# Performance work log

Measured on AMD Instinct MI355X. Metric: run time of the kernel, lower is better.

## Reference

```python
import jax, jax.numpy as jnp
import numpy as np

C, G, NH, NE = 640, 32, 8, 512
B, H, W, P = 8, 32, 32, 77
HD = C // NH
EPS = 1e-5


def _groupnorm(x, g, b):
    # x: (B, C, H, W); normalize over (C//G, H, W) within each of G groups
    bb, cc, hh, ww = x.shape
    xg = x.reshape(bb, G, cc // G, hh, ww)
    mu = xg.mean(axis=(2, 3, 4), keepdims=True)
    var = xg.var(axis=(2, 3, 4), keepdims=True)
    xg = (xg - mu) * jax.lax.rsqrt(var + EPS)
    return xg.reshape(bb, cc, hh, ww) * g[None, :, None, None] + b[None, :, None, None]


def _layernorm(x, g, b):
    mu = x.mean(axis=-1, keepdims=True)
    var = x.var(axis=-1, keepdims=True)
    return (x - mu) * jax.lax.rsqrt(var + EPS) * g + b


def _split_heads(t):
    # (B, S, C) -> (B, NH, S, HD)
    bb, ss, _ = t.shape
    return t.reshape(bb, ss, NH, HD).transpose(0, 2, 1, 3)


def _attn(q, k, v):
    # q,k,v: (B, NH, S, HD) — manual softmax(q k^T / sqrt(d)) v, as in the source
    scores = jnp.einsum('bhqd,bhkd->bhqk', q, k) / (HD ** 0.5)
    probs = jax.nn.softmax(scores, axis=-1)
    out = jnp.einsum('bhqk,bhkd->bhqd', probs, v)
    bb = q.shape[0]
    return out.transpose(0, 2, 1, 3).reshape(bb, q.shape[2], C)


def unet_attention_fwd(x, p, gn_g, gn_b, ci_w, ci_b, ln1_g, ln1_b,
                       qkv_w, qkv_b, saw_w, saw_b, ln2_g, ln2_b,
                       caq_w, caq_b, cak_w, cak_b, cav_w, cav_b, caw_w, caw_b,
                       ln3_g, ln3_b, g1_w, g1_b, g2_w, g2_b, co_w, co_b):
    residue_long = x
    h = _groupnorm(x, gn_g, gn_b)
    # conv_input: 1x1 conv == per-pixel linear; ci_w: (C_in, C_out)
    h = jnp.einsum('bihw,io->bohw', h, ci_w) + ci_b[None, :, None, None]
    bb, cc, hh, ww = h.shape
    h = h.reshape(bb, cc, hh * ww).transpose(0, 2, 1)  # (B, HW, C)

    # self attention
    res = h
    t = _layernorm(h, ln1_g, ln1_b)
    qkv = t @ qkv_w + qkv_b
    q, k, v = jnp.split(qkv, 3, axis=-1)
    t = _attn(_split_heads(q), _split_heads(k), _split_heads(v))
    h = res + (t @ saw_w + saw_b)

    # cross attention (prompt p: (B, 77, NE))
    res = h
    t = _layernorm(h, ln2_g, ln2_b)
    q = t @ caq_w + caq_b
    k = p @ cak_w + cak_b
    v = p @ cav_w + cav_b
    t = _attn(_split_heads(q), _split_heads(k), _split_heads(v))
    h = res + (t @ caw_w + caw_b)

    # GEGLU MLP (exact GELU, matching torch F.gelu default)
    res = h
    t = _layernorm(h, ln3_g, ln3_b)
    proj = t @ g1_w + g1_b  # (B, HW, 8C)
    a, gate = jnp.split(proj, 2, axis=-1)
    t = a * jax.nn.gelu(gate, approximate=False)
    h = res + (t @ g2_w + g2_b)

    h = h.transpose(0, 2, 1).reshape(bb, cc, hh, ww)
    out = jnp.einsum('bihw,io->bohw', h, co_w) + co_b[None, :, None, None]
    return out + residue_long


def setup_inputs() -> dict:
    keys = jax.random.split(jax.random.key(0), 20)
    ki = iter(keys)
    s = 0.02

    def w(shape):
        return jax.random.normal(next(ki), shape, jnp.float32) * s

    return {
        'x': jax.random.normal(next(ki), (B, C, H, W), jnp.float32),
        'p': jax.random.normal(next(ki), (B, P, NE), jnp.float32),
        'gn_g': jnp.ones((C,), jnp.float32), 'gn_b': jnp.zeros((C,), jnp.float32),
        'ci_w': w((C, C)), 'ci_b': jnp.zeros((C,), jnp.float32),
        'ln1_g': jnp.ones((C,), jnp.float32), 'ln1_b': jnp.zeros((C,), jnp.float32),
        'qkv_w': w((C, 3 * C)), 'qkv_b': jnp.zeros((3 * C,), jnp.float32),
        'saw_w': w((C, C)), 'saw_b': jnp.zeros((C,), jnp.float32),
        'ln2_g': jnp.ones((C,), jnp.float32), 'ln2_b': jnp.zeros((C,), jnp.float32),
        'caq_w': w((C, C)), 'caq_b': jnp.zeros((C,), jnp.float32),
        'cak_w': w((NE, C)), 'cak_b': jnp.zeros((C,), jnp.float32),
        'cav_w': w((NE, C)), 'cav_b': jnp.zeros((C,), jnp.float32),
        'caw_w': w((C, C)), 'caw_b': jnp.zeros((C,), jnp.float32),
        'ln3_g': jnp.ones((C,), jnp.float32), 'ln3_b': jnp.zeros((C,), jnp.float32),
        'g1_w': w((C, 8 * C)), 'g1_b': jnp.zeros((8 * C,), jnp.float32),
        'g2_w': w((4 * C, C)), 'g2_b': jnp.zeros((C,), jnp.float32),
        'co_w': w((C, C)), 'co_b': jnp.zeros((C,), jnp.float32),
    }


def reference(x, p, gn_g, gn_b, ci_w, ci_b, ln1_g, ln1_b,
              qkv_w, qkv_b, saw_w, saw_b, ln2_g, ln2_b,
              caq_w, caq_b, cak_w, cak_b, cav_w, cav_b, caw_w, caw_b,
              ln3_g, ln3_b, g1_w, g1_b, g2_w, g2_b, co_w, co_b):
    return unet_attention_fwd(x, p, gn_g, gn_b, ci_w, ci_b, ln1_g, ln1_b,
                              qkv_w, qkv_b, saw_w, saw_b, ln2_g, ln2_b,
                              caq_w, caq_b, cak_w, cak_b, cav_w, cav_b, caw_w, caw_b,
                              ln3_g, ln3_b, g1_w, g1_b, g2_w, g2_b, co_w, co_b)
```

## Files before the change

### kernel.cpp

```cpp
#include <hip/hip_runtime.h>
#include <math.h>

typedef unsigned short u16;
typedef __attribute__((ext_vector_type(8))) short short8;
typedef __attribute__((ext_vector_type(4))) float f32x4;

#define DI static __device__ __forceinline__

DI float bf2f(u16 u) { union { unsigned u; float f; } c; c.u = (unsigned)u << 16; return c.f; }
DI u16 f2bf(float f) {
  union { float f; unsigned u; } c; c.f = f;
  unsigned r = c.u + 0x7fffu + ((c.u >> 16) & 1u);
  return (u16)(r >> 16);
}

DI void gload16(const u16* g, u16* l) {
  __builtin_amdgcn_global_load_lds(
      (const __attribute__((address_space(1))) unsigned int*)g,
      (__attribute__((address_space(3))) unsigned int*)l, 16, 0, 0);
}

DI void xcd_swz(int& bx, int& by, int gx, int gy) {
  int id = by * gx + bx;
  int n = gx * gy;
  int q = n >> 3, r = n & 7;
  int xcd = id & 7, k = id >> 3;
  int s = (xcd < r) ? (xcd * (q + 1) + k) : (r * (q + 1) + (xcd - r) * q + k);
  bx = s % gx;
  by = s / gx;
}

DI void xcd_swz_rect(int& bx, int& by, int gx, int gy) {
  if ((gx & 7) == 0) {
    int RC = gx >> 3;
    if (RC <= 8 && (8 % RC) == 0) {
      int RR = 8 / RC;
      if ((gy % RR) == 0) {
        int id = by * gx + bx;
        int xcd = id & 7, k = id >> 3;
        int rc = xcd % RC, rr = xcd / RC;
        int RH = gy / RR;
        bx = rc * 8 + (k & 7);
        by = rr * RH + (k >> 3);
        return;
      }
    }
  }
  xcd_swz(bx, by, gx, gy);
}

DI const short8* fragp(const u16* unit, int row, int g4) {
  int off = row * 64 + g4 * 16;
  off ^= ((off >> 7) & 3) << 4;
  return (const short8*)((const char*)unit + off);
}

struct PrepDesc { const float* src; u16* dst; int K, N, nbx, boff, perm; };
struct PrepArgs { PrepDesc d[10]; };

__global__ __launch_bounds__(256) void prep_all(PrepArgs a) {
  int bid = blockIdx.x;
  int i = 0;
  while (i < 9 && bid >= a.d[i + 1].boff) i++;
  const PrepDesc D = a.d[i];
  int rel = bid - D.boff;
  int bx = rel % D.nbx, by = rel / D.nbx;
  int K = D.K, N = D.N;
  __shared__ float tile[32][33];
  int k0 = by * 32, n0 = bx * 32;
  int tid = threadIdx.x;
  int ni = tid & 31, ki8 = tid >> 5;
  for (int q = 0; q < 4; q++) {
    int k = ki8 + q * 8;
    tile[k][ni] = D.src[(size_t)(k0 + k) * N + n0 + ni];
  }
  __syncthreads();
  int kj = tid & 31, nj8 = tid >> 5;
  for (int q = 0; q < 4; q++) {
    int n = nj8 + q * 8;
    int nold = n0 + n;
    int rowp = nold;
    if (D.perm) {
      rowp = (nold < 2560) ? ((nold >> 5) * 64 + (nold & 31))
                           : (((nold - 2560) >> 5) * 64 + 32 + (nold & 31));
    }
    D.dst[(size_t)rowp * K + k0 + kj] = f2bf(tile[kj][n]);
  }
}

__global__ __launch_bounds__(256) void conv_bf16(const float* __restrict__ in,
                                                 u16* __restrict__ out, long n) {
  long i = (long)blockIdx.x * 256 + threadIdx.x;
  if (i < n) out[i] = f2bf(in[i]);
}

__global__ __launch_bounds__(256) void concat2(const float* __restrict__ a,
                                               const float* __restrict__ b,
                                               float* __restrict__ o, int n) {
  int i = blockIdx.x * 256 + threadIdx.x;
  if (i < n) o[i] = a[i];
  else if (i < 2 * n) o[i] = b[i - n];
}

__global__ __launch_bounds__(256) void gn_stats(const float* __restrict__ x,
                                                float* __restrict__ mean_o,
                                                float* __restrict__ rstd_o) {
  int bg = blockIdx.x;
  const float4* p = (const float4*)(x + (size_t)bg * 20480);
  float s = 0.f, sq = 0.f;
  for (int i = threadIdx.x; i < 5120; i += 256) {
    float4 v = p[i];
    s += v.x + v.y + v.z + v.w;
    sq += v.x * v.x + v.y * v.y + v.z * v.z + v.w * v.w;
  }
  for (int off = 1; off < 64; off <<= 1) { s += __shfl_xor(s, off); sq += __shfl_xor(sq, off); }
  __shared__ float ps[4], pq[4];
  int w = threadIdx.x >> 6;
  if ((threadIdx.x & 63) == 0) { ps[w] = s; pq[w] = sq; }
  __syncthreads();
  if (threadIdx.x == 0) {
    float S = ps[0] + ps[1] + ps[2] + ps[3];
    float Q = pq[0] + pq[1] + pq[2] + pq[3];
    float mu = S / 20480.f;
    float var = Q / 20480.f - mu * mu;
    mean_o[bg] = mu;
    rstd_o[bg] = rsqrtf(var + 1e-5f);
  }
}

__global__ __launch_bounds__(256) void gn_apply(const float* __restrict__ x,
                                                const float* __restrict__ mean_,
                                                const float* __restrict__ rstd_,
                                                const float* __restrict__ g,
                                                const float* __restrict__ bb,
                                                u16* __restrict__ out) {
  __shared__ float tile[32][33];
  int b = blockIdx.z, c0 = blockIdx.y * 32, s0 = blockIdx.x * 32;
  int tid = threadIdx.x;
  int si = tid & 31, ci8 = tid >> 5;
  for (int i = 0; i < 4; i++) {
    int c = c0 + ci8 + i * 8;
    int gg = c / 20;
    float mu = mean_[b * 32 + gg], rs = rstd_[b * 32 + gg];
    float v = x[((size_t)b * 640 + c) * 1024 + s0 + si];
    tile[ci8 + i * 8][si] = (v - mu) * rs * g[c] + bb[c];
  }
  __syncthreads();
  int cj = tid & 31, sj8 = tid >> 5;
  for (int i = 0; i < 4; i++) {
    int sj = sj8 + i * 8;
    out[((size_t)b * 1024 + s0 + sj) * 640 + c0 + cj] = f2bf(tile[cj][sj]);
  }
}

__global__ __launch_bounds__(256) void ln_kernel(const float* __restrict__ in,
                                                 const float* __restrict__ g,
                                                 const float* __restrict__ bb,
                                                 u16* __restrict__ out) {
  int t = blockIdx.x * 4 + (threadIdx.x >> 6);
  int lane = threadIdx.x & 63;
  const float* row = in + (size_t)t * 640;
  float xv[10], s = 0.f, sq = 0.f;
  for (int j = 0; j < 10; j++) {
    xv[j] = row[lane + j * 64];
    s += xv[j];
    sq += xv[j] * xv[j];
  }
  for (int off = 1; off < 64; off <<= 1) { s += __shfl_xor(s, off); sq += __shfl_xor(sq, off); }
  float mu = s * (1.f / 640.f);
  float var = sq * (1.f / 640.f) - mu * mu;
  float rstd = rsqrtf(var + 1e-5f);
  for (int j = 0; j < 10; j++) {
    int c = lane + j * 64;
    out[(size_t)t * 640 + c] = f2bf((xv[j] - mu) * rstd * g[c] + bb[c]);
  }
}

template <int MODE>
DI void store_elem(void* outp, const float* res, size_t o, float val) {
  if (MODE == 0)
    ((float*)outp)[o] = val;
  else if (MODE == 1)
    ((u16*)outp)[o] = f2bf(val);
  else if (MODE == 2)
    ((float*)outp)[o] = val + res[o];
  else
    ((u16*)outp)[o] = f2bf(val + res[o]);
}

template <int MODE>
__global__ __launch_bounds__(512, 1) void gemm256(const u16* __restrict__ A,
                                                  const u16* __restrict__ Bt,
                                                  const float* __restrict__ bias,
                                                  void* outp, const float* res,
                                                  int M, int N, int K) {
  __shared__ __align__(16) u16 As[4][8192];
  __shared__ __align__(16) u16 Bs[4][8192];
  const int tid = threadIdx.x;
  const int lane = tid & 63, wid = tid >> 6;
  const int wm = wid >> 2, wn = wid & 3;
  const int rq = lane & 15, g4 = lane >> 4;
  int bx = blockIdx.x, by = blockIdx.y;
  xcd_swz_rect(bx, by, gridDim.x, gridDim.y);
  const int m0 = bx * 256, n0 = by * 256;

  int D0 = tid * 16;
  int so = D0 ^ (((D0 >> 7) & 3) << 4);
  const int srow = so >> 6;
  const int sk16 = (so & 63) >> 1;

  f32x4 acc[8][4] = {};
  const int nt = K >> 5;

#define STG_A(kt)                                                              \
  {                                                                            \
    gload16(A + (size_t)(m0 + srow) * K + (kt)*32 + sk16,                      \
            &As[(kt) & 3][0] + tid * 8);                                       \
    gload16(A + (size_t)(m0 + 128 + srow) * K + (kt)*32 + sk16,                \
            &As[(kt) & 3][4096] + tid * 8);                                    \
  }
#define STG_B(kt)                                                              \
  {                                                                            \
    gload16(Bt + (size_t)(n0 + srow) * K + (kt)*32 + sk16,                     \
            &Bs[(kt) & 3][0] + tid * 8);                                       \
    gload16(Bt + (size_t)(n0 + 128 + srow) * K + (kt)*32 + sk16,               \
            &Bs[(kt) & 3][4096] + tid * 8);                                    \
  }
#define BAR asm volatile("s_barrier" ::: "memory")

#define PH1(T)                                                                 \
  {                                                                            \
    const u16* Au = &As[(T) & 3][0];                                           \
    const u16* Bu = &Bs[(T) & 3][0];                                           \
    _Pragma("unroll") for (int i = 0; i < 4; i++)                              \
        af[i] = *fragp(Au, wm * 128 + i * 16 + rq, g4);                        \
    _Pragma("unroll") for (int j = 0; j < 4; j++)                              \
        bf[j] = *fragp(Bu, wn * 64 + j * 16 + rq, g4);                         \
    BAR;                                                                       \
    asm volatile("s_waitcnt lgkmcnt(0)" ::: "memory");                         \
    __builtin_amdgcn_sched_barrier(0);                                         \
    __builtin_amdgcn_s_setprio(1);                                             \
    _Pragma("unroll") for (int i = 0; i < 4; i++)                              \
        _Pragma("unroll") for (int j = 0; j < 4; j++)                          \
            acc[i][j] =                                                        \
        __builtin_amdgcn_mfma_f32_16x16x32_bf16(af[i], bf[j], acc[i][j], 0, 0, 0); \
    __builtin_amdgcn_s_setprio(0);                                             \
  }

#define PH2(T, DO_STG, WSTR)                                                   \
  {                                                                            \
    const u16* Au = &As[(T) & 3][0];                                           \
    _Pragma("unroll") for (int i = 0; i < 4; i++)                              \
        af[i] = *fragp(Au, wm * 128 + 64 + i * 16 + rq, g4);                   \
    if (DO_STG) { STG_A((T) + 3); STG_B((T) + 3); }                            \
    asm volatile(WSTR ::: "memory");                                           \
    BAR;                                                                       \
    asm volatile("s_waitcnt lgkmcnt(0)" ::: "memory");                         \
    __builtin_amdgcn_sched_barrier(0);                                         \
    __builtin_amdgcn_s_setprio(1);                                             \
    _Pragma("unroll") for (int i = 0; i < 4; i++)                              \
        _Pragma("unroll") for (int j = 0; j < 4; j++)                          \
            acc[4 + i][j] =                                                    \
        __builtin_amdgcn_mfma_f32_16x16x32_bf16(af[i], bf[j], acc[4 + i][j], 0, 0, 0); \
    __builtin_amdgcn_s_setprio(0);                                             \
  }

  STG_A(0); STG_B(0); STG_A(1); STG_B(1); STG_A(2); STG_B(2);
  asm volatile("s_waitcnt vmcnt(8)" ::: "memory");
  BAR;

  short8 af[4], bf[4];
  int t = 0;
  for (; t < nt - 3; t++) {
    PH1(t);
    PH2(t, true, "s_waitcnt vmcnt(8)");
  }
  PH1(t); PH2(t, false, "s_waitcnt vmcnt(4)"); t++;
  PH1(t); PH2(t, false, "s_waitcnt vmcnt(0)"); t++;
  PH1(t); PH2(t, false, "s_nop 0");

  if (MODE == 5) {
#pragma unroll
    for (int mf = 0; mf < 8; mf++) {
      int mb = m0 + wm * 128 + mf * 16 + g4 * 4;
#pragma unroll
      for (int j = 0; j < 2; j++) {
        int n = n0 + wn * 64 + j * 16 + rq;
        int c = (n >> 6) * 32 + (n & 31);
        float ba = bias[c];
        float bg = bias[2560 + c];
#pragma unroll
        for (int r = 0; r < 4; r++) {
          float a = acc[mf][j][r] + ba;
          float gt = acc[mf][j + 2][r] + bg;
          float gl = 0.5f * gt * (1.f + erff(gt * 0.70710678f));
          ((u16*)outp)[(size_t)(mb + r) * 2560 + c] = f2bf(a * gl);
        }
      }
    }
  } else {
#pragma unroll
    for (int mf = 0; mf < 8; mf++) {
#pragma unroll
      for (int j = 0; j < 4; j++) {
        int n = n0 + wn * 64 + j * 16 + rq;
        if (n >= N) continue;
        float bv = bias[n];
        int mb = m0 + wm * 128 + mf * 16 + g4 * 4;
        f32x4 v = acc[mf][j];
#pragma unroll
        for (int r = 0; r < 4; r++) {
          size_t o = (size_t)(mb + r) * N + n;
          ((u16*)outp)[o] = f2bf(v[r] + bv);
        }
      }
    }
  }
  (void)res;
#undef STG_A
#undef STG_B
#undef PH1
#undef PH2
#undef BAR
}

template <int MODE>
__global__ __launch_bounds__(256) void gemm_bt64(const u16* __restrict__ A,
                                                 const u16* __restrict__ Bt,
                                                 const float* __restrict__ bias,
                                                 void* outp, const float* res,
                                                 int M, int N, int K) {
  __shared__ __align__(16) u16 As[4][2048];
  __shared__ __align__(16) u16 Bs[4][4096];
  const int tid = threadIdx.x;
  const int lane = tid & 63, wid = tid >> 6;
  const int wm = wid >> 1, wn = wid & 1;
  int bx = blockIdx.x, by = blockIdx.y;
  xcd_swz(bx, by, gridDim.x, gridDim.y);
  const int m0 = bx * 64, n0 = by * 128;
  const int rq = lane & 15, g4 = lane >> 4;

  int D0 = tid * 16;
  int so = D0 ^ (((D0 >> 7) & 3) << 4);
  const int srowS = so >> 6;
  const int sk16 = (so & 63) >> 1;
  int gmA = m0 + srowS;  if (gmA >= M) gmA = M - 1;
  const u16* gA = A + (size_t)gmA * K + sk16;
  const u16* gB0 = Bt + (size_t)(n0 + srowS) * K + sk16;
  const u16* gB1 = Bt + (size_t)(n0 + 64 + srowS) * K + sk16;

  f32x4 acc[2][4] = {};

  auto STAGE = [&](int buf, int k0) {
    gload16(gA + k0, &As[buf][tid * 8]);
    gload16(gB0 + k0, &Bs[buf][tid * 8]);
    gload16(gB1 + k0, &Bs[buf][2048 + tid * 8]);
  };
  auto COMPUTE = [&](int buf) {
    short8 af[2], bfr[4];
    for (int i = 0; i < 2; i++)
      af[i] = *fragp(&As[buf][0], wm * 32 + i * 16 + rq, g4);
    for (int j = 0; j < 4; j++)
      bfr[j] = *fragp(&Bs[buf][0], wn * 64 + j * 16 + rq, g4);
    __builtin_amdgcn_s_setprio(1);
    for (int i = 0; i < 2; i++)
      for (int j = 0; j < 4; j++)
        acc[i][j] = __builtin_amdgcn_mfma_f32_16x16x32_bf16(af[i], bfr[j], acc[i][j], 0, 0, 0);
    __builtin_amdgcn_s_setprio(0);
  };

  const int nk = K >> 5;
  STAGE(0, 0);
  STAGE(1, 32);
  int t = 0;
  for (; t < nk - 2; t++) {
    STAGE((t + 2) & 3, (t + 2) << 5);
    asm volatile("s_waitcnt vmcnt(6)" ::: "memory");
    __builtin_amdgcn_s_barrier();
    COMPUTE(t & 3);
  }
  asm volatile("s_waitcnt vmcnt(3)" ::: "memory");
  __builtin_amdgcn_s_barrier();
  COMPUTE(t & 3);
  t++;
  asm volatile("s_waitcnt vmcnt(0)" ::: "memory");
  __builtin_amdgcn_s_barrier();
  COMPUTE(t & 3);

  for (int j = 0; j < 4; j++) {
    int n = n0 + wn * 64 + j * 16 + rq;
    float bv = bias[n];
    for (int i = 0; i < 2; i++) {
      int mb = m0 + wm * 32 + i * 16 + g4 * 4;
      f32x4 v = acc[i][j];
      if (MODE == 3) {
        int b = mb >> 10, sp = mb & 1023;
        size_t o = ((size_t)b * 640 + n) * 1024 + sp;
        f32x4 xv = *(const f32x4*)(res + o);
        f32x4 ov;
        for (int r = 0; r < 4; r++) ov[r] = v[r] + bv + xv[r];
        *(f32x4*)((float*)outp + o) = ov;
      } else {
        for (int r = 0; r < 4; r++) {
          int m = mb + r;
          if (m >= M) break;
          store_elem<MODE>(outp, res, (size_t)m * N + n, v[r] + bv);
        }
      }
    }
  }
}

__global__ __launch_bounds__(256) void attn_kernel(const u16* __restrict__ Qb, int ldq, long qbs,
                                                   const u16* __restrict__ Kb, int ldk, long kbs,
                                                   const u16* __restrict__ Vb,
                                                   u16* __restrict__ Ob, int ldo, long obs,
                                                   int Sk, float scale) {
  __shared__ __align__(16) u16 Ks[64 * 96];
  __shared__ __align__(16) u16 Vt[80 * 64];
  __shared__ __align__(16) u16 Ps[4][16 * 72];
  const short8 zero = {0, 0, 0, 0, 0, 0, 0, 0};
  const int tid = threadIdx.x;
  const int lane = tid & 63, w = tid >> 6;
  const int rq = lane & 15, g4 = lane >> 4;
  const int b = blockIdx.z, h = blockIdx.y;
  const u16* Q = Qb + (size_t)b * qbs + h * 80;
  const u16* Kp = Kb + (size_t)b * kbs + h * 80;
  const u16* Vp = Vb + (size_t)b * kbs + h * 80;
  u16* Op = Ob + (size_t)b * obs + h * 80;
  const int q0 = blockIdx.x * 64 + w * 16;
  const float Af = scale * 1.44269504f;

  short8 qa[3];
#pragma unroll
  for (int kk = 0; kk < 3; kk++) {
    int d = kk * 32 + g4 * 8;
    qa[kk] = (d < 80) ? *(const short8*)(Q + (size_t)(q0 + rq) * ldq + d) : zero;
  }
  f32x4 oacc[5] = {};
  float m_run = -1e30f, l_run = 0.f;

  const int nkt = (Sk + 63) >> 6;
  for (int kt = 0; kt < nkt; kt++) {
    const int kbase = kt * 64;
    for (int s = tid; s < 768; s += 256) {
      int row = s / 12, c = s % 12;
      int kidx = kbase + row;
      short8 v = zero;
      if (c < 10 && kidx < Sk) v = *(const short8*)(Kp + (size_t)kidx * ldk + c * 8);
      int byte = row * 192 + c * 16;
      byte ^= (row & 7) << 4;
      *(short8*)((char*)Ks + byte) = v;
    }
    for (int s = tid; s < 320; s += 256) {
      int k2 = (s & 31) * 2, c = s >> 5;
      int k0i = kbase + k2;
      short8 v0 = zero, v1 = zero;
      if (k0i < Sk) v0 = *(const short8*)(Vp + (size_t)k0i * ldk + c * 8);
      if (k0i + 1 < Sk) v1 = *(const short8*)(Vp + (size_t)(k0i + 1) * ldk + c * 8);
#pragma unroll
      for (int jj = 0; jj < 8; jj++) {
        int d = c * 8 + jj;
        unsigned cm = (unsigned)(u16)v0[jj] | ((unsigned)(u16)v1[jj] << 16);
        int byte = d * 128 + k2 * 2;
        byte ^= (d & 7) << 4;
        *(unsigned*)((char*)Vt + byte) = cm;
      }
    }
    __syncthreads();

    f32x4 sc[4] = {};
#pragma unroll
    for (int n = 0; n < 4; n++)
#pragma unroll
      for (int kk = 0; kk < 3; kk++) {
        int row = n * 16 + rq;
        int byte = row * 192 + (kk * 32 + g4 * 8) * 2;
        byte ^= (rq & 7) << 4;
        short8 kb = *(const short8*)((const char*)Ks + byte);
        sc[n] = __builtin_amdgcn_mfma_f32_16x16x32_bf16(kb, qa[kk], sc[n], 0, 0, 0);
      }
    const bool full = (kbase + 64 <= Sk);
    if (!full) {
#pragma unroll
      for (int n = 0; n < 4; n++)
#pragma unroll
        for (int r = 0; r < 4; r++)
          if (kbase + n * 16 + g4 * 4 + r >= Sk) sc[n][r] = -1e30f;
    }
    float t0 = fmaxf(fmaxf(sc[0][0], sc[0][1]), fmaxf(sc[0][2], sc[0][3]));
    float t1 = fmaxf(fmaxf(sc[1][0], sc[1][1]), fmaxf(sc[1][2], sc[1][3]));
    float t2 = fmaxf(fmaxf(sc[2][0], sc[2][1]), fmaxf(sc[2][2], sc[2][3]));
    float t3 = fmaxf(fmaxf(sc[3][0], sc[3][1]), fmaxf(sc[3][2], sc[3][3]));
    float tm = fmaxf(fmaxf(t0, t1), fmaxf(t2, t3));
    tm = fmaxf(tm, __shfl_xor(tm, 16));
    tm = fmaxf(tm, __shfl_xor(tm, 32));
    if (!__all(tm <= m_run + 48.0f)) {
      float mn = fmaxf(m_run, tm);
      float sf = exp2f(Af * (m_run - mn));
      m_run = mn;
      l_run *= sf;
      float sfo[4];
#pragma unroll
      for (int r = 0; r < 4; r++) sfo[r] = __shfl(sf, g4 * 4 + r);
#pragma unroll
      for (int nn = 0; nn < 5; nn++)
#pragma unroll
        for (int r = 0; r < 4; r++) oacc[nn][r] *= sfo[r];
    }
    const float Am = Af * m_run;
    float rs0 = 0.f, rs1 = 0.f;
#pragma unroll
    for (int n = 0; n < 4; n++) {
      float p0 = exp2f(fmaf(Af, sc[n][0], -Am));
      float p1 = exp2f(fmaf(Af, sc[n][1], -Am));
      float p2 = exp2f(fmaf(Af, sc[n][2], -Am));
      float p3 = exp2f(fmaf(Af, sc[n][3], -Am));
      sc[n][0] = p0; sc[n][1] = p1; sc[n][2] = p2; sc[n][3] = p3;
      rs0 += p0 + p1;
      rs1 += p2 + p3;
    }
    float rsum = rs0 + rs1;
    rsum += __shfl_xor(rsum, 16);
    rsum += __shfl_xor(rsum, 32);
    l_run += rsum;
#pragma unroll
    for (int n = 0; n < 4; n++) {
      unsigned pk0, pk1;
      asm("v_cvt_pk_bf16_f32 %0, %1, %2" : "=v"(pk0) : "v"(sc[n][0]), "v"(sc[n][1]));
      asm("v_cvt_pk_bf16_f32 %0, %1, %2" : "=v"(pk1) : "v"(sc[n][2]), "v"(sc[n][3]));
      int base = rq * 72 + n * 16 + g4 * 4;
      *(unsigned*)&Ps[w][base] = pk0;
      *(unsigned*)&Ps[w][base + 2] = pk1;
    }
    __builtin_amdgcn_s_setprio(1);
#pragma unroll
    for (int s = 0; s < 2; s++) {
      short8 pa = *(const short8*)&Ps[w][rq * 72 + s * 32 + g4 * 8];
#pragma unroll
      for (int nn = 0; nn < 5; nn++) {
        int row = nn * 16 + rq;
        int byte = row * 128 + (s * 32 + g4 * 8) * 2;
        byte ^= (rq & 7) << 4;
        short8 vb = *(const short8*)((const char*)Vt + byte);
        oacc[nn] = __builtin_amdgcn_mfma_f32_16x16x32_bf16(pa, vb, oacc[nn], 0, 0, 0);
      }
    }
    __builtin_amdgcn_s_setprio(0);
    __syncthreads();
  }
  float lo[4];
#pragma unroll
  for (int r = 0; r < 4; r++) lo[r] = 1.0f / __shfl(l_run, g4 * 4 + r);
#pragma unroll
  for (int nn = 0; nn < 5; nn++)
#pragma unroll
    for (int r = 0; r < 4; r++)
      Op[(size_t)(q0 + g4 * 4 + r) * ldo + nn * 16 + rq] = f2bf(oacc[nn][r] * lo[r]);
}

extern "C" void kernel_launch(void* const* d_in, const int* in_sizes, int n_in,
                              void* d_out, int out_size, void* d_ws, size_t ws_size,
                              hipStream_t stream) {
  (void)in_sizes; (void)n_in; (void)out_size; (void)ws_size;
  const float* x = (const float*)d_in[0];
  const float* p = (const float*)d_in[1];
  const float* gn_g = (const float*)d_in[2];
  const float* gn_b = (const float*)d_in[3];
  const float* ci_w = (const float*)d_in[4];
  const float* ci_b = (const float*)d_in[5];
  const float* ln1_g = (const float*)d_in[6];
  const float* ln1_b = (const float*)d_in[7];
  const float* qkv_w = (const float*)d_in[8];
  const float* qkv_b = (const float*)d_in[9];
  const float* saw_w = (const float*)d_in[10];
  const float* saw_b = (const float*)d_in[11];
  const float* ln2_g = (const float*)d_in[12];
  const float* ln2_b = (const float*)d_in[13];
  const float* caq_w = (const float*)d_in[14];
  const float* caq_b = (const float*)d_in[15];
  const float* cak_w = (const float*)d_in[16];
  const float* cak_b = (const float*)d_in[17];
  const float* cav_w = (const float*)d_in[18];
  const float* cav_b = (const float*)d_in[19];
  const float* caw_w = (const float*)d_in[20];
  const float* caw_b = (const float*)d_in[21];
  const float* ln3_g = (const float*)d_in[22];
  const float* ln3_b = (const float*)d_in[23];
  const float* g1_w = (const float*)d_in[24];
  const float* g1_b = (const float*)d_in[25];
  const float* g2_w = (const float*)d_in[26];
  const float* g2_b = (const float*)d_in[27];
  const float* co_w = (const float*)d_in[28];
  const float* co_b = (const float*)d_in[29];
  float* out = (float*)d_out;

  char* ws = (char*)d_ws;
  size_t off = 0;
  auto alloc = [&](size_t bytes) {
    size_t o = off;
    off += (bytes + 255) & ~(size_t)255;
    return o;
  };
  u16* WCI = (u16*)(ws + alloc((size_t)768 * 640 * 2));
  u16* WQKV = (u16*)(ws + alloc((size_t)2048 * 640 * 2));
  u16* WSAW = (u16*)(ws + alloc((size_t)768 * 640 * 2));
  u16* WCAQ = (u16*)(ws + alloc((size_t)768 * 640 * 2));
  u16* WCAKV = (u16*)(ws + alloc((size_t)1280 * 512 * 2));
  u16* WCAW = (u16*)(ws + alloc((size_t)768 * 640 * 2));
  u16* WG1 = (u16*)(ws + alloc((size_t)5120 * 640 * 2));
  u16* WG2 = (u16*)(ws + alloc((size_t)768 * 2560 * 2));
  u16* WCO = (u16*)(ws + alloc((size_t)768 * 640 * 2));
  u16* X = (u16*)(ws + alloc((size_t)8192 * 640 * 2));
  u16* Y = (u16*)(ws + alloc((size_t)8192 * 640 * 2));
  float* F1 = (float*)(ws + alloc((size_t)8192 * 640 * 4));
  u16* QKV = (u16*)(ws + alloc((size_t)8192 * 1920 * 2));
  u16* PBF = (u16*)(ws + alloc((size_t)616 * 512 * 2));
  u16* KVC = (u16*)(ws + alloc((size_t)616 * 1280 * 2));
  u16* TG = (u16*)(ws + alloc((size_t)8192 * 2560 * 2));
  float* GNM = (float*)(ws + alloc(256 * 4));
  float* GNR = (float*)(ws + alloc(256 * 4));
  float* CBIAS = (float*)(ws + alloc(1280 * 4));

  PrepArgs pa;
  int boff = 0;
  auto addw = [&](int idx, const float* src, u16* dst, int K, int N, int perm) {
    pa.d[idx].src = src; pa.d[idx].dst = dst;
    pa.d[idx].K = K; pa.d[idx].N = N;
    pa.d[idx].nbx = N / 32; pa.d[idx].boff = boff; pa.d[idx].perm = perm;
    boff += (N / 32) * (K / 32);
  };
  addw(0, ci_w, WCI, 640, 640, 0);
  addw(1, qkv_w, WQKV, 640, 1920, 0);
  addw(2, saw_w, WSAW, 640, 640, 0);
  addw(3, caq_w, WCAQ, 640, 640, 0);
  addw(4, cak_w, WCAKV, 512, 640, 0);
  addw(5, cav_w, WCAKV + (size_t)640 * 512, 512, 640, 0);
  addw(6, caw_w, WCAW, 640, 640, 0);
  addw(7, g1_w, WG1, 640, 5120, 1);
  addw(8, g2_w, WG2, 2560, 640, 0);
  addw(9, co_w, WCO, 640, 640, 0);
  prep_all<<<boff, 256, 0, stream>>>(pa);
  conv_bf16<<<1232, 256, 0, stream>>>(p, PBF, (long)616 * 512);
  concat2<<<5, 256, 0, stream>>>(cak_b, cav_b, CBIAS, 640);

  gn_stats<<<256, 256, 0, stream>>>(x, GNM, GNR);
  gn_apply<<<dim3(32, 20, 8), 256, 0, stream>>>(x, GNM, GNR, gn_g, gn_b, X);

  const float scale = 0.11180339887498949f;

  gemm_bt64<0><<<dim3(128, 5), 256, 0, stream>>>(X, WCI, ci_b, F1, nullptr, 8192, 640, 640);
  ln_kernel<<<2048, 256, 0, stream>>>(F1, ln1_g, ln1_b, Y);
  gemm256<1><<<dim3(32, 8), 512, 0, stream>>>(Y, WQKV, qkv_b, QKV, nullptr, 8192, 1920, 640);
  attn_kernel<<<dim3(16, 8, 8), 256, 0, stream>>>(QKV, 1920, (long)1024 * 1920,
                                                  QKV + 640, 1920, (long)1024 * 1920,
                                                  QKV + 1280, X, 640, (long)1024 * 640,
                                                  1024, scale);
  gemm_bt64<2><<<dim3(128, 5), 256, 0, stream>>>(X, WSAW, saw_b, F1, F1, 8192, 640, 640);
  ln_kernel<<<2048, 256, 0, stream>>>(F1, ln2_g, ln2_b, Y);
  gemm_bt64<1><<<dim3(128, 5), 256, 0, stream>>>(Y, WCAQ, caq_b, X, nullptr, 8192, 640, 640);
  gemm_bt64<1><<<dim3(10, 10), 256, 0, stream>>>(PBF, WCAKV, CBIAS, KVC, nullptr, 616, 1280, 512);
  attn_kernel<<<dim3(16, 8, 8), 256, 0, stream>>>(X, 640, (long)1024 * 640,
                                                  KVC, 1280, (long)77 * 1280,
                                                  KVC + 640, Y, 640, (long)1024 * 640,
                                                  77, scale);
  gemm_bt64<2><<<dim3(128, 5), 256, 0, stream>>>(Y, WCAW, caw_b, F1, F1, 8192, 640, 640);
  ln_kernel<<<2048, 256, 0, stream>>>(F1, ln3_g, ln3_b, X);
  gemm256<5><<<dim3(32, 20), 512, 0, stream>>>(X, WG1, g1_b, TG, nullptr, 8192, 5120, 640);
  gemm_bt64<4><<<dim3(128, 5), 256, 0, stream>>>(TG, WG2, g2_b, X, F1, 8192, 640, 2560);
  gemm_bt64<3><<<dim3(128, 5), 256, 0, stream>>>(X, WCO, co_b, out, x, 8192, 640, 640);
}
```

Measured before the change: 445.2 us.

## Run GEGLU GEMM on new 128x128 tile kernel with supertile block swizzle

Adds a gemm_bt kernel that uses 128x128 tiles, 256 threads, a 4-buffer LDS ring and a fused GEGLU epilogue. It replaces the 256-tile, 512-thread gemm256 for the large G1 projection. Blocks are remapped into 8x8 supertiles to improve L2 reuse of A and B. The GEGLU epilogue is removed from gemm256, trading larger-tile reuse for more blocks and a simpler pipeline.

```diff
diff --git a/kernel.cpp b/kernel.cpp
--- a/kernel.cpp
+++ b/kernel.cpp
@@ -45,6 +45,19 @@
         return;
       }
     }
+  }
+  xcd_swz(bx, by, gx, gy);
+}
+
+DI void supertile_swz(int& bx, int& by, int gx, int gy) {
+  if ((gx & 7) == 0 && (gy & 7) == 0) {
+    int id = by * gx + bx;
+    int s = id >> 6, w = id & 63;
+    int syn = gy >> 3;
+    int sy = s % syn, sx = s / syn;
+    bx = sx * 8 + (w & 7);
+    by = sy * 8 + (w >> 3);
+    return;
   }
   xcd_swz(bx, by, gx, gy);
 }
@@ -279,40 +292,19 @@
   PH1(t); PH2(t, false, "s_waitcnt vmcnt(0)"); t++;
   PH1(t); PH2(t, false, "s_nop 0");
 
-  if (MODE == 5) {
-#pragma unroll
-    for (int mf = 0; mf < 8; mf++) {
+#pragma unroll
+  for (int mf = 0; mf < 8; mf++) {
+#pragma unroll
+    for (int j = 0; j < 4; j++) {
+      int n = n0 + wn * 64 + j * 16 + rq;
+      if (n >= N) continue;
+      float bv = bias[n];
       int mb = m0 + wm * 128 + mf * 16 + g4 * 4;
-#pragma unroll
-      for (int j = 0; j < 2; j++) {
-        int n = n0 + wn * 64 + j * 16 + rq;
-        int c = (n >> 6) * 32 + (n & 31);
-        float ba = bias[c];
-        float bg = bias[2560 + c];
-#pragma unroll
-        for (int r = 0; r < 4; r++) {
-          float a = acc[mf][j][r] + ba;
-          float gt = acc[mf][j + 2][r] + bg;
-          float gl = 0.5f * gt * (1.f + erff(gt * 0.70710678f));
-          ((u16*)outp)[(size_t)(mb + r) * 2560 + c] = f2bf(a * gl);
-        }
-      }
-    }
-  } else {
-#pragma unroll
-    for (int mf = 0; mf < 8; mf++) {
-#pragma unroll
-      for (int j = 0; j < 4; j++) {
-        int n = n0 + wn * 64 + j * 16 + rq;
-        if (n >= N) continue;
-        float bv = bias[n];
-        int mb = m0 + wm * 128 + mf * 16 + g4 * 4;
-        f32x4 v = acc[mf][j];
-#pragma unroll
-        for (int r = 0; r < 4; r++) {
-          size_t o = (size_t)(mb + r) * N + n;
-          ((u16*)outp)[o] = f2bf(v[r] + bv);
-        }
+      f32x4 v = acc[mf][j];
+#pragma unroll
+      for (int r = 0; r < 4; r++) {
+        size_t o = (size_t)(mb + r) * N + n;
+        ((u16*)outp)[o] = f2bf(v[r] + bv);
       }
     }
   }
@@ -322,6 +314,117 @@
 #undef PH1
 #undef PH2
 #undef BAR
+}
+
+template <int MODE>
+__global__ __launch_bounds__(256) void gemm_bt(const u16* __restrict__ A,
+                                               const u16* __restrict__ Bt,
+                                               const float* __restrict__ bias,
+                                               void* outp, const float* res,
+                                               int M, int N, int K) {
+  __shared__ __align__(16) u16 As[4][4096];
+  __shared__ __align__(16) u16 Bs[4][4096];
+  const int tid = threadIdx.x;
+  const int lane = tid & 63, wid = tid >> 6;
+  const int wm = wid >> 1, wn = wid & 1;
+  int bx = blockIdx.x, by = blockIdx.y;
+  supertile_swz(bx, by, gridDim.x, gridDim.y);
+  const int m0 = bx * 128, n0 = by * 128;
+  const int rq = lane & 15, g4 = lane >> 4;
+
+  int D0 = tid * 16;
+  int so = D0 ^ (((D0 >> 7) & 3) << 4);
+  const int srowS = so >> 6;
+  const int sk16 = (so & 63) >> 1;
+  int gmA0 = m0 + srowS;       if (gmA0 >= M) gmA0 = M - 1;
+  int gmA1 = m0 + 64 + srowS;  if (gmA1 >= M) gmA1 = M - 1;
+  const u16* gA0 = A + (size_t)gmA0 * K + sk16;
+  const u16* gA1 = A + (size_t)gmA1 * K + sk16;
+  const u16* gB0 = Bt + (size_t)(n0 + srowS) * K + sk16;
+  const u16* gB1 = Bt + (size_t)(n0 + 64 + srowS) * K + sk16;
+
+  f32x4 acc[4][4] = {};
+
+  auto STAGE = [&](int buf, int k0) {
+    gload16(gA0 + k0, &As[buf][tid * 8]);
+    gload16(gA1 + k0, &As[buf][2048 + tid * 8]);
+    gload16(gB0 + k0, &Bs[buf][tid * 8]);
+    gload16(gB1 + k0, &Bs[buf][2048 + tid * 8]);
+  };
+  auto COMPUTE = [&](int buf) {
+    short8 af[4], bfr[4];
+    for (int i = 0; i < 4; i++)
+      af[i] = *fragp(&As[buf][0], wm * 64 + i * 16 + rq, g4);
+    for (int j = 0; j < 4; j++)
+      bfr[j] = *fragp(&Bs[buf][0], wn * 64 + j * 16 + rq, g4);
+    __builtin_amdgcn_s_setprio(1);
+    for (int i = 0; i < 4; i++)
+      for (int j = 0; j < 4; j++)
+        acc[i][j] = __builtin_amdgcn_mfma_f32_16x16x32_bf16(af[i], bfr[j], acc[i][j], 0, 0, 0);
+    __builtin_amdgcn_s_setprio(0);
+  };
+
+  const int nk = K >> 5;
+  STAGE(0, 0);
+  STAGE(1, 32);
+  int t = 0;
+  for (; t < nk - 2; t++) {
+    STAGE((t + 2) & 3, (t + 2) << 5);
+    asm volatile("s_waitcnt vmcnt(8)" ::: "memory");
+    __builtin_amdgcn_s_barrier();
+    COMPUTE(t & 3);
+  }
+  asm volatile("s_waitcnt vmcnt(4)" ::: "memory");
+  __builtin_amdgcn_s_barrier();
+  COMPUTE(t & 3);
+  t++;
+  asm volatile("s_waitcnt vmcnt(0)" ::: "memory");
+  __builtin_amdgcn_s_barrier();
+  COMPUTE(t & 3);
+
+  if (MODE == 5) {
+#pragma unroll
+    for (int i = 0; i < 4; i++) {
+      int mb = m0 + wm * 64 + i * 16 + g4 * 4;
+#pragma unroll
+      for (int j = 0; j < 2; j++) {
+        int n = n0 + wn * 64 + j * 16 + rq;
+        int c = (n >> 6) * 32 + (n & 31);
+        float ba = bias[c];
+        float bg = bias[2560 + c];
+#pragma unroll
+        for (int r = 0; r < 4; r++) {
+          float a = acc[i][j][r] + ba;
+          float gt = acc[i][j + 2][r] + bg;
+          float gl = 0.5f * gt * (1.f + erff(gt * 0.70710678f));
+          ((u16*)outp)[(size_t)(mb + r) * 2560 + c] = f2bf(a * gl);
+        }
+      }
+    }
+    return;
+  }
+  for (int j = 0; j < 4; j++) {
+    int n = n0 + wn * 64 + j * 16 + rq;
+    float bv = bias[n];
+    for (int i = 0; i < 4; i++) {
+      int mb = m0 + wm * 64 + i * 16 + g4 * 4;
+      f32x4 v = acc[i][j];
+      if (MODE == 3) {
+        int b = mb >> 10, sp = mb & 1023;
+        size_t o = ((size_t)b * 640 + n) * 1024 + sp;
+        f32x4 xv = *(const f32x4*)(res + o);
+        f32x4 ov;
+        for (int r = 0; r < 4; r++) ov[r] = v[r] + bv + xv[r];
+        *(f32x4*)((float*)outp + o) = ov;
+      } else {
+        for (int r = 0; r < 4; r++) {
+          int m = mb + r;
+          if (m >= M) break;
+          store_elem<MODE>(outp, res, (size_t)m * N + n, v[r] + bv);
+        }
+      }
+    }
+  }
 }
 
 template <int MODE>
@@ -666,7 +769,7 @@
                                                   77, scale);
   gemm_bt64<2><<<dim3(128, 5), 256, 0, stream>>>(Y, WCAW, caw_b, F1, F1, 8192, 640, 640);
   ln_kernel<<<2048, 256, 0, stream>>>(F1, ln3_g, ln3_b, X);
-  gemm256<5><<<dim3(32, 20), 512, 0, stream>>>(X, WG1, g1_b, TG, nullptr, 8192, 5120, 640);
+  gemm_bt<5><<<dim3(64, 40), 256, 0, stream>>>(X, WG1, g1_b, TG, nullptr, 8192, 5120, 640);
   gemm_bt64<4><<<dim3(128, 5), 256, 0, stream>>>(TG, WG2, g2_b, X, F1, 8192, 640, 2560);
   gemm_bt64<3><<<dim3(128, 5), 256, 0, stream>>>(X, WCO, co_b, out, x, 8192, 640, 640);
 }
```

Measured after the change: 462.6 us. +3.9%, slower.
